# Kernel optimization log

Measured on AMD Instinct MI355X. Metric: run time of the kernel, lower is better.

The kernel has to match this reference:

```python
import jax, jax.numpy as jnp
import numpy as np


def _ragged_reverse(x, lengths):
    # x: [N, L, C]; flip the first `lengths[n]` steps of each sample, zero-fill the rest.
    N, L, C = x.shape
    t = jnp.arange(L, dtype=lengths.dtype)[None, :]          # [1, L]
    Ln = lengths[:, None]                                     # [N, 1]
    valid = t < Ln                                            # [N, L]
    idx = jnp.where(valid, Ln - 1 - t, 0)                     # [N, L]
    rev = jnp.take_along_axis(x, idx[:, :, None], axis=1)     # [N, L, C]
    return jnp.where(valid[:, :, None], rev, jnp.zeros((), x.dtype))


def _gru(xb, W_ih, W_hh, b_ih, b_hh):
    # xb: [B, L, C] -> outputs [B, L, H] (standard torch GRU cell math).
    B, L, C = xb.shape
    H = W_hh.shape[0]
    xw = xb @ W_ih + b_ih                                     # [B, L, 3H], input proj done once

    def step(h, xw_t):
        gh = h @ W_hh + b_hh                                  # [B, 3H]
        xr, xz, xn = jnp.split(xw_t, 3, axis=-1)
        hr, hz, hn = jnp.split(gh, 3, axis=-1)
        r = jax.nn.sigmoid(xr + hr)
        z = jax.nn.sigmoid(xz + hz)
        n = jnp.tanh(xn + r * hn)
        h_new = (1.0 - z) * n + z * h
        return h_new, h_new

    h0 = jnp.zeros((B, H), xb.dtype)
    _, ys = jax.lax.scan(step, h0, jnp.swapaxes(xw, 0, 1))    # ys: [L, B, H]
    return jnp.swapaxes(ys, 0, 1)                             # [B, L, H]


def reference(x, lengths, W_ih, W_hh, b_ih, b_hh):
    N, L, C = x.shape
    # to_bidirection: stack [forward; ragged-reversed] along batch -> [2N, L, C]
    rev = _ragged_reverse(x, lengths)
    xb = jnp.concatenate([x, rev], axis=0)
    out = _gru(xb, W_ih, W_hh, b_ih, b_hh)                    # [2N, L, H]
    # from_bidirection: split halves, concat on feature dim -> [N, L, 2H]
    return jnp.concatenate([out[:N], out[N:]], axis=2)


def setup_inputs() -> dict:
    key = jax.random.key(0)
    ks = jax.random.split(key, 6)
    N, L, C, H = 32, 2048, 64, 128
    s = 1.0 / np.sqrt(H)
    return {
        "x": jax.random.normal(ks[0], (N, L, C), dtype=jnp.float32),
        "lengths": jax.random.randint(ks[1], (N,), 1, L + 1, dtype=jnp.int32),
        "W_ih": jax.random.normal(ks[2], (C, 3 * H), dtype=jnp.float32) * s,
        "W_hh": jax.random.normal(ks[3], (H, 3 * H), dtype=jnp.float32) * s,
        "b_ih": jax.random.normal(ks[4], (3 * H,), dtype=jnp.float32) * s,
        "b_hh": jax.random.normal(ks[5], (3 * H,), dtype=jnp.float32) * s,
    }
```

## Files before the change

kernel.cpp:

```cpp
#include <hip/hip_runtime.h>

#define L_SEQ 2048
#define C_IN  64
#define HH    128
#define NSEQ  32
#define B2    64
#define G3    384
#define RING  16

typedef _Float16 half2_t __attribute__((ext_vector_type(2)));

#define PINU(v) asm volatile("" : "+v"(v))
#define STEP_BARRIER() asm volatile("s_waitcnt lgkmcnt(0)\n\ts_barrier" ::: "memory")

__device__ __forceinline__ float fdot2u(unsigned int a, unsigned int b, float c) {
    return __builtin_amdgcn_fdot2(__builtin_bit_cast(half2_t, a),
                                  __builtin_bit_cast(half2_t, b), c, false);
}

__device__ __forceinline__ unsigned int pack_h2(float a, float b) {
    half2_t t; t.x = (_Float16)a; t.y = (_Float16)b;
    return __builtin_bit_cast(unsigned int, t);
}

__device__ __forceinline__ float qadd1(float x) {
    int t = __builtin_amdgcn_update_dpp(0, __builtin_bit_cast(int, x),
                                        0xB1, 0xF, 0xF, true);
    return x + __builtin_bit_cast(float, t);
}

__device__ __forceinline__ float fast_sigmoid(float x) {
    float e = __builtin_amdgcn_exp2f(-1.4426950408889634f * x);
    return __builtin_amdgcn_rcpf(1.0f + e);
}

__device__ __forceinline__ float fast_tanh(float x) {
    float a = fabsf(x);
    float e = __builtin_amdgcn_exp2f(-2.8853900817779268f * a);
    float r = (1.0f - e) * __builtin_amdgcn_rcpf(1.0f + e);
    return copysignf(r, x);
}

__device__ __forceinline__ float pdot32(const unsigned int (&w)[32],
                                        const unsigned int* xrow, float acc) {
    const uint4* x4 = (const uint4*)xrow;
#pragma unroll
    for (int i = 0; i < 8; ++i) {
        const uint4 v = x4[i];
        acc = fdot2u(v.x, w[4*i+0], acc);
        acc = fdot2u(v.y, w[4*i+1], acc);
        acc = fdot2u(v.z, w[4*i+2], acc);
        acc = fdot2u(v.w, w[4*i+3], acc);
    }
    return acc;
}

__global__ __launch_bounds__(512) __attribute__((amdgpu_waves_per_eu(1, 1)))
void bigru_fused(const float* __restrict__ x, const int* __restrict__ lengths,
                 const float* __restrict__ W_ih, const float* __restrict__ W_hh,
                 const float* __restrict__ b_ih, const float* __restrict__ b_hh,
                 float* __restrict__ out)
{
    __shared__ unsigned int hbufu[2][64];
    __shared__ float        ring[RING][G3];
    __shared__ unsigned int xstage[2][2][32];

    const int tid = threadIdx.x;
    const int s   = blockIdx.x;
    const bool isFwd = (s < NSEQ);
    const int  len   = isFwd ? L_SEQ : lengths[s - NSEQ];
    const float* __restrict__ xseq = x + (size_t)(s % NSEQ) * L_SEQ * C_IN;

    const bool consumer = (tid < 256);
    const int u = tid & 255;
    const int j = u >> 1;
    const int p = u & 1;

    unsigned int w0[32], w1[32], w2[32];
    float bA = 0.f, bB = 0.f;

    if (consumer) {
        const float* Wb = W_hh + (size_t)(64 * p) * G3;
#pragma unroll
        for (int k = 0; k < 32; ++k) {
            w0[k] = pack_h2(Wb[(2*k) * G3 + j],       Wb[(2*k+1) * G3 + j]);
            w1[k] = pack_h2(Wb[(2*k) * G3 + 128 + j], Wb[(2*k+1) * G3 + 128 + j]);
            w2[k] = pack_h2(Wb[(2*k) * G3 + 256 + j], Wb[(2*k+1) * G3 + 256 + j]);
        }
#pragma unroll
        for (int k = 0; k < 32; ++k) { PINU(w0[k]); PINU(w1[k]); PINU(w2[k]); }
        bA = b_hh[256 + j];
        if (tid < 64) hbufu[0][tid] = 0u;
    } else {
#pragma unroll
        for (int k = 0; k < 32; ++k)
            w0[k] = pack_h2(W_ih[(2*k) * G3 + u], W_ih[(2*k+1) * G3 + u]);
        bA = b_ih[u] + b_hh[u];
        if (u >= 128) {
            const int c1 = 128 + u;
#pragma unroll
            for (int k = 0; k < 32; ++k)
                w1[k] = pack_h2(W_ih[(2*k) * G3 + c1], W_ih[(2*k+1) * G3 + c1]);
            bB = b_ih[c1];
        }
#pragma unroll
        for (int k = 0; k < 32; ++k) { PINU(w0[k]); PINU(w1[k]); }
    }

    float2 xv = make_float2(0.f, 0.f);

    for (int pg = 0; pg < 4; ++pg) {
        if (!consumer && u < 64) {
            const int rowIdx = 2 * pg + (u >= 32 ? 1 : 0);
            const int e = u & 31;
            const int srcL = isFwd ? rowIdx : (len - 1 - rowIdx);
            float2 v = make_float2(0.f, 0.f);
            if (srcL >= 0) v = *(const float2*)&xseq[(size_t)srcL * C_IN + 2*e];
            xstage[pg & 1][(u >= 32) ? 1 : 0][e] = pack_h2(v.x, v.y);
        }
        __syncthreads();
        if (!consumer && pg < 3) {
            const unsigned int* xsA = &xstage[pg & 1][0][0];
            const unsigned int* xsB = &xstage[pg & 1][1][0];
            ring[2*pg][u]     = pdot32(w0, xsA, bA);
            ring[2*pg + 1][u] = pdot32(w0, xsB, bA);
            if (u >= 128) {
                ring[2*pg][128 + u]     = pdot32(w1, xsA, bB);
                ring[2*pg + 1][128 + u] = pdot32(w1, xsB, bB);
            }
        }
        __syncthreads();
    }

    float cr = 0.f, cz = 0.f, cn = 0.f, nr = 0.f, nz = 0.f, nn = 0.f;
    float hreg = 0.f;
    if (consumer) { cr = ring[0][j]; cz = ring[0][128 + j]; cn = ring[0][256 + j]; }

    float* outbase = out + (size_t)(s % NSEQ) * L_SEQ * 256 + (isFwd ? 0 : HH);
    int cur = 0;

    for (int g = 0; g < L_SEQ / 2; ++g) {
        const int tA = 2 * g;
        if (consumer) {
            const int sln = (tA + 1) & (RING - 1);
            nr = ring[sln][j]; nz = ring[sln][128 + j]; nn = ring[sln][256 + j];
            float ar = 0.f, az = 0.f, an = 0.f;
            const uint4* hb = (const uint4*)&hbufu[cur][p * 32];
#pragma unroll
            for (int i = 0; i < 8; ++i) {
                const uint4 hv = hb[i];
                ar = fdot2u(hv.x, w0[4*i+0], ar); ar = fdot2u(hv.y, w0[4*i+1], ar);
                ar = fdot2u(hv.z, w0[4*i+2], ar); ar = fdot2u(hv.w, w0[4*i+3], ar);
                az = fdot2u(hv.x, w1[4*i+0], az); az = fdot2u(hv.y, w1[4*i+1], az);
                az = fdot2u(hv.z, w1[4*i+2], az); az = fdot2u(hv.w, w1[4*i+3], az);
                an = fdot2u(hv.x, w2[4*i+0], an); an = fdot2u(hv.y, w2[4*i+1], an);
                an = fdot2u(hv.z, w2[4*i+2], an); an = fdot2u(hv.w, w2[4*i+3], an);
            }
            ar = qadd1(ar); az = qadd1(az); an = qadd1(an);
            const float r = fast_sigmoid(cr + ar);
            const float z = fast_sigmoid(cz + az);
            const float n = fast_tanh(cn + r * (an + bA));
            const float hnew = z * (hreg - n) + n;
            hreg = hnew;
            if (p == 0) {
                ((_Float16*)&hbufu[cur ^ 1][0])[j] = (_Float16)hnew;
                outbase[(size_t)tA * 256 + j] = hnew;
            }
            cur ^= 1;
        } else {
            const int rdA = tA + 6;
            if (rdA < L_SEQ) {
                const unsigned int* xsA = &xstage[(g + 1) & 1][0][0];
                const unsigned int* xsB = &xstage[(g + 1) & 1][1][0];
                const int slA = rdA & (RING - 1), slB = (rdA + 1) & (RING - 1);
                ring[slA][u] = pdot32(w0, xsA, bA);
                ring[slB][u] = pdot32(w0, xsB, bA);
                if (u >= 128) {
                    ring[slA][128 + u] = pdot32(w1, xsA, bB);
                    ring[slB][128 + u] = pdot32(w1, xsB, bB);
                }
            }
            const int rl = tA + 8;
            if (u < 64 && rl < L_SEQ) {
                const int rowIdx = rl + (u >= 32 ? 1 : 0);
                const int e = u & 31;
                const int srcL = isFwd ? rowIdx : (len - 1 - rowIdx);
                xv = make_float2(0.f, 0.f);
                if (srcL >= 0) xv = *(const float2*)&xseq[(size_t)srcL * C_IN + 2*e];
            }
        }
        STEP_BARRIER();
        {
            const int tB = tA + 1;
            if (consumer) {
                const int sln = (tB + 1) & (RING - 1);
                cr = ring[sln][j]; cz = ring[sln][128 + j]; cn = ring[sln][256 + j];
                float ar = 0.f, az = 0.f, an = 0.f;
                const uint4* hb = (const uint4*)&hbufu[cur][p * 32];
#pragma unroll
                for (int i = 0; i < 8; ++i) {
                    const uint4 hv = hb[i];
                    ar = fdot2u(hv.x, w0[4*i+0], ar); ar = fdot2u(hv.y, w0[4*i+1], ar);
                    ar = fdot2u(hv.z, w0[4*i+2], ar); ar = fdot2u(hv.w, w0[4*i+3], ar);
                    az = fdot2u(hv.x, w1[4*i+0], az); az = fdot2u(hv.y, w1[4*i+1], az);
                    az = fdot2u(hv.z, w1[4*i+2], az); az = fdot2u(hv.w, w1[4*i+3], az);
                    an = fdot2u(hv.x, w2[4*i+0], an); an = fdot2u(hv.y, w2[4*i+1], an);
                    an = fdot2u(hv.z, w2[4*i+2], an); an = fdot2u(hv.w, w2[4*i+3], an);
                }
                ar = qadd1(ar); az = qadd1(az); an = qadd1(an);
                const float r = fast_sigmoid(nr + ar);
                const float z = fast_sigmoid(nz + az);
                const float n = fast_tanh(nn + r * (an + bA));
                const float hnew = z * (hreg - n) + n;
                hreg = hnew;
                if (p == 0) {
                    ((_Float16*)&hbufu[cur ^ 1][0])[j] = (_Float16)hnew;
                    outbase[(size_t)tB * 256 + j] = hnew;
                }
                cur ^= 1;
            } else {
                if (u < 64 && tA + 8 < L_SEQ) {
                    xstage[g & 1][(u >= 32) ? 1 : 0][u & 31] = pack_h2(xv.x, xv.y);
                }
            }
        }
        STEP_BARRIER();
    }
}

extern "C" void kernel_launch(void* const* d_in, const int* in_sizes, int n_in,
                              void* d_out, int out_size, void* d_ws, size_t ws_size,
                              hipStream_t stream) {
    const float* x       = (const float*)d_in[0];
    const int*   lengths = (const int*)  d_in[1];
    const float* W_ih    = (const float*)d_in[2];
    const float* W_hh    = (const float*)d_in[3];
    const float* b_ih    = (const float*)d_in[4];
    const float* b_hh    = (const float*)d_in[5];
    float* out = (float*)d_out;

    bigru_fused<<<dim3(B2), dim3(512), 0, stream>>>(
        x, lengths, W_ih, W_hh, b_ih, b_hh, out);
}
```

Measured before the change: 1.151 ms.

## Pre-pack input to fp16 in a separate kernel and read rows directly from global

Adds a pre-pass kernel that converts x to packed half2 in workspace, plus a zero row for out-of-range reversed indices. The producer waves then read x rows straight from global/L2 for the input projection, which removes the LDS staging buffer and the two-barrier pipelined loop. The recurrence loop becomes one step per iteration with one barrier. The cost is an extra kernel launch and global-load latency on the producer path. The producer now depends on each uniform global load landing in time, since it stays only 6 steps ahead.

```diff
diff --git a/kernel.cpp b/kernel.cpp
--- a/kernel.cpp
+++ b/kernel.cpp
@@ -7,6 +7,8 @@
 #define B2    64
 #define G3    384
 #define RING  16
+#define XW32  (C_IN / 2)
+#define XTOT  (NSEQ * L_SEQ * XW32)
 
 typedef _Float16 half2_t __attribute__((ext_vector_type(2)));
 
@@ -42,7 +44,8 @@
 }
 
 __device__ __forceinline__ float pdot32(const unsigned int (&w)[32],
-                                        const unsigned int* xrow, float acc) {
+                                        const unsigned int* __restrict__ xrow,
+                                        float acc) {
     const uint4* x4 = (const uint4*)xrow;
 #pragma unroll
     for (int i = 0; i < 8; ++i) {
@@ -55,21 +58,33 @@
     return acc;
 }
 
+__global__ __launch_bounds__(256)
+void pack_x_kernel(const float* __restrict__ x, unsigned int* __restrict__ xh)
+{
+    const size_t i = (size_t)blockIdx.x * 256 + threadIdx.x;
+    if (i < (size_t)XTOT) {
+        const float2 v = ((const float2*)x)[i];
+        xh[i] = pack_h2(v.x, v.y);
+    }
+    if (i < XW32) xh[(size_t)XTOT + i] = 0u;
+}
+
 __global__ __launch_bounds__(512) __attribute__((amdgpu_waves_per_eu(1, 1)))
-void bigru_fused(const float* __restrict__ x, const int* __restrict__ lengths,
+void bigru_fused(const unsigned int* __restrict__ xh,
+                 const int* __restrict__ lengths,
                  const float* __restrict__ W_ih, const float* __restrict__ W_hh,
                  const float* __restrict__ b_ih, const float* __restrict__ b_hh,
                  float* __restrict__ out)
 {
     __shared__ unsigned int hbufu[2][64];
     __shared__ float        ring[RING][G3];
-    __shared__ unsigned int xstage[2][2][32];
 
     const int tid = threadIdx.x;
     const int s   = blockIdx.x;
     const bool isFwd = (s < NSEQ);
     const int  len   = isFwd ? L_SEQ : lengths[s - NSEQ];
-    const float* __restrict__ xseq = x + (size_t)(s % NSEQ) * L_SEQ * C_IN;
+    const unsigned int* __restrict__ xseq = xh + (size_t)(s % NSEQ) * L_SEQ * XW32;
+    const unsigned int* __restrict__ zrow = xh + (size_t)XTOT;
 
     const bool consumer = (tid < 256);
     const int u = tid & 255;
@@ -105,45 +120,29 @@
         }
 #pragma unroll
         for (int k = 0; k < 32; ++k) { PINU(w0[k]); PINU(w1[k]); }
-    }
-
-    float2 xv = make_float2(0.f, 0.f);
-
-    for (int pg = 0; pg < 4; ++pg) {
-        if (!consumer && u < 64) {
-            const int rowIdx = 2 * pg + (u >= 32 ? 1 : 0);
-            const int e = u & 31;
-            const int srcL = isFwd ? rowIdx : (len - 1 - rowIdx);
-            float2 v = make_float2(0.f, 0.f);
-            if (srcL >= 0) v = *(const float2*)&xseq[(size_t)srcL * C_IN + 2*e];
-            xstage[pg & 1][(u >= 32) ? 1 : 0][e] = pack_h2(v.x, v.y);
-        }
-        __syncthreads();
-        if (!consumer && pg < 3) {
-            const unsigned int* xsA = &xstage[pg & 1][0][0];
-            const unsigned int* xsB = &xstage[pg & 1][1][0];
-            ring[2*pg][u]     = pdot32(w0, xsA, bA);
-            ring[2*pg + 1][u] = pdot32(w0, xsB, bA);
-            if (u >= 128) {
-                ring[2*pg][128 + u]     = pdot32(w1, xsA, bB);
-                ring[2*pg + 1][128 + u] = pdot32(w1, xsB, bB);
-            }
-        }
-        __syncthreads();
-    }
-
-    float cr = 0.f, cz = 0.f, cn = 0.f, nr = 0.f, nz = 0.f, nn = 0.f;
-    float hreg = 0.f;
+
+        for (int rd = 0; rd < 6; ++rd) {
+            const int srcL = isFwd ? rd : (len - 1 - rd);
+            const unsigned int* xrow =
+                (srcL >= 0) ? (xseq + (size_t)srcL * XW32) : zrow;
+            ring[rd][u] = pdot32(w0, xrow, bA);
+            if (u >= 128) ring[rd][128 + u] = pdot32(w1, xrow, bB);
+        }
+    }
+    __syncthreads();
+
+    float cr = 0.f, cz = 0.f, cn = 0.f, hreg = 0.f;
     if (consumer) { cr = ring[0][j]; cz = ring[0][128 + j]; cn = ring[0][256 + j]; }
 
     float* outbase = out + (size_t)(s % NSEQ) * L_SEQ * 256 + (isFwd ? 0 : HH);
     int cur = 0;
 
-    for (int g = 0; g < L_SEQ / 2; ++g) {
-        const int tA = 2 * g;
+    for (int t = 0; t < L_SEQ; ++t) {
         if (consumer) {
-            const int sln = (tA + 1) & (RING - 1);
-            nr = ring[sln][j]; nz = ring[sln][128 + j]; nn = ring[sln][256 + j];
+            const int sln = (t + 1) & (RING - 1);
+            const float nr = ring[sln][j];
+            const float nz = ring[sln][128 + j];
+            const float nn = ring[sln][256 + j];
             float ar = 0.f, az = 0.f, an = 0.f;
             const uint4* hb = (const uint4*)&hbufu[cur][p * 32];
 #pragma unroll
@@ -164,64 +163,19 @@
             hreg = hnew;
             if (p == 0) {
                 ((_Float16*)&hbufu[cur ^ 1][0])[j] = (_Float16)hnew;
-                outbase[(size_t)tA * 256 + j] = hnew;
+                outbase[(size_t)t * 256 + j] = hnew;
             }
             cur ^= 1;
+            cr = nr; cz = nz; cn = nn;
         } else {
-            const int rdA = tA + 6;
-            if (rdA < L_SEQ) {
-                const unsigned int* xsA = &xstage[(g + 1) & 1][0][0];
-                const unsigned int* xsB = &xstage[(g + 1) & 1][1][0];
-                const int slA = rdA & (RING - 1), slB = (rdA + 1) & (RING - 1);
-                ring[slA][u] = pdot32(w0, xsA, bA);
-                ring[slB][u] = pdot32(w0, xsB, bA);
-                if (u >= 128) {
-                    ring[slA][128 + u] = pdot32(w1, xsA, bB);
-                    ring[slB][128 + u] = pdot32(w1, xsB, bB);
-                }
-            }
-            const int rl = tA + 8;
-            if (u < 64 && rl < L_SEQ) {
-                const int rowIdx = rl + (u >= 32 ? 1 : 0);
-                const int e = u & 31;
-                const int srcL = isFwd ? rowIdx : (len - 1 - rowIdx);
-                xv = make_float2(0.f, 0.f);
-                if (srcL >= 0) xv = *(const float2*)&xseq[(size_t)srcL * C_IN + 2*e];
-            }
-        }
-        STEP_BARRIER();
-        {
-            const int tB = tA + 1;
-            if (consumer) {
-                const int sln = (tB + 1) & (RING - 1);
-                cr = ring[sln][j]; cz = ring[sln][128 + j]; cn = ring[sln][256 + j];
-                float ar = 0.f, az = 0.f, an = 0.f;
-                const uint4* hb = (const uint4*)&hbufu[cur][p * 32];
-#pragma unroll
-                for (int i = 0; i < 8; ++i) {
-                    const uint4 hv = hb[i];
-                    ar = fdot2u(hv.x, w0[4*i+0], ar); ar = fdot2u(hv.y, w0[4*i+1], ar);
-                    ar = fdot2u(hv.z, w0[4*i+2], ar); ar = fdot2u(hv.w, w0[4*i+3], ar);
-                    az = fdot2u(hv.x, w1[4*i+0], az); az = fdot2u(hv.y, w1[4*i+1], az);
-                    az = fdot2u(hv.z, w1[4*i+2], az); az = fdot2u(hv.w, w1[4*i+3], az);
-                    an = fdot2u(hv.x, w2[4*i+0], an); an = fdot2u(hv.y, w2[4*i+1], an);
-                    an = fdot2u(hv.z, w2[4*i+2], an); an = fdot2u(hv.w, w2[4*i+3], an);
-                }
-                ar = qadd1(ar); az = qadd1(az); an = qadd1(an);
-                const float r = fast_sigmoid(nr + ar);
-                const float z = fast_sigmoid(nz + az);
-                const float n = fast_tanh(nn + r * (an + bA));
-                const float hnew = z * (hreg - n) + n;
-                hreg = hnew;
-                if (p == 0) {
-                    ((_Float16*)&hbufu[cur ^ 1][0])[j] = (_Float16)hnew;
-                    outbase[(size_t)tB * 256 + j] = hnew;
-                }
-                cur ^= 1;
-            } else {
-                if (u < 64 && tA + 8 < L_SEQ) {
-                    xstage[g & 1][(u >= 32) ? 1 : 0][u & 31] = pack_h2(xv.x, xv.y);
-                }
+            const int rd = t + 6;
+            if (rd < L_SEQ) {
+                const int srcL = isFwd ? rd : (len - 1 - rd);
+                const unsigned int* xrow =
+                    (srcL >= 0) ? (xseq + (size_t)srcL * XW32) : zrow;
+                const int sl = rd & (RING - 1);
+                ring[sl][u] = pdot32(w0, xrow, bA);
+                if (u >= 128) ring[sl][128 + u] = pdot32(w1, xrow, bB);
             }
         }
         STEP_BARRIER();
@@ -239,6 +193,9 @@
     const float* b_hh    = (const float*)d_in[5];
     float* out = (float*)d_out;
 
+    unsigned int* xh = (unsigned int*)d_ws;
+
+    pack_x_kernel<<<dim3((XTOT + 255) / 256), dim3(256), 0, stream>>>(x, xh);
     bigru_fused<<<dim3(B2), dim3(512), 0, stream>>>(
-        x, lengths, W_ih, W_hh, b_ih, b_hh, out);
-}
+        xh, lengths, W_ih, W_hh, b_ih, b_hh, out);
+}
```

Measured after the change: 1.149 ms. About the same (-0.2%).
